# Performance work log

Measured on AMD Instinct MI355X. Metric: run time of the kernel, lower is better.

Reference implementation:

```python
import jax, jax.numpy as jnp
import numpy as np

B, T, F, U, M = 4096, 16, 256, 512, 8
DELTA_T = 0.04

# ln_tau_table: tau = 1, 10^0.5, 10^1.0, ... -> ln(tau) = i * 0.5*ln(10)
LN_TAU = (jnp.arange(M, dtype=jnp.float32) * (0.5 * np.log(10.0))).astype(jnp.float32)
DECAY = jnp.exp(-DELTA_T / (LN_TAU + 1e-7))  # [M]


def setup_inputs() -> dict:
    key = jax.random.key(0)
    ks = jax.random.split(key, 9)
    s = lambda fan_in: 1.0 / np.sqrt(fan_in)
    return {
        "x": jax.random.normal(ks[0], (B, T, F), dtype=jnp.float32),
        "W_r": jax.random.normal(ks[1], (F + U, U * M), dtype=jnp.float32) * s(F + U),
        "b_r": jax.random.normal(ks[2], (U * M,), dtype=jnp.float32) * 0.01,
        "W_q": jax.random.normal(ks[3], (F + U, U), dtype=jnp.float32) * s(F + U),
        "b_q": jax.random.normal(ks[4], (U,), dtype=jnp.float32) * 0.01,
        "W_s": jax.random.normal(ks[5], (F + U, U * M), dtype=jnp.float32) * s(F + U),
        "b_s": jax.random.normal(ks[6], (U * M,), dtype=jnp.float32) * 0.01,
        "W_out": jax.random.normal(ks[7], (U, 3), dtype=jnp.float32) * s(U),
        "b_out": jax.random.normal(ks[8], (3,), dtype=jnp.float32) * 0.01,
    }


def _ctgru_forward(x, W_r, b_r, W_q, b_q, W_s, b_s, W_out, b_out):
    def step(h_hat, x_t):  # h_hat: [B,U,M], x_t: [B,F]
        h = h_hat.sum(axis=2)                              # [B,U]
        fused = jnp.concatenate([x_t, h], axis=1)          # [B,F+U]
        ln_tau_r = (fused @ W_r + b_r).reshape(-1, U, M)   # [B,U,M]
        r_ki = jax.nn.softmax(-jnp.square(ln_tau_r - LN_TAU), axis=2)
        q_in = jnp.concatenate([x_t, jnp.sum(r_ki * h_hat, axis=2)], axis=1)
        q_k = jnp.tanh(q_in @ W_q + b_q)[:, :, None]       # [B,U,1]
        ln_tau_s = (fused @ W_s + b_s).reshape(-1, U, M)
        s_ki = jax.nn.softmax(-jnp.square(ln_tau_s - LN_TAU), axis=2)
        h_next = ((1.0 - s_ki) * h_hat + s_ki * q_k) * DECAY
        return h_next, h_next.sum(axis=2)                  # carry, hidden [B,U]

    h0 = jnp.zeros((x.shape[0], U, M), dtype=x.dtype)
    _, hiddens = jax.lax.scan(step, h0, jnp.swapaxes(x, 0, 1))  # hiddens: [T,B,U]
    outputs = jnp.swapaxes(hiddens, 0, 1)                  # [B,T,U]
    return outputs @ W_out + b_out                         # [B,T,3]


def reference(x, W_r, b_r, W_q, b_q, W_s, b_s, W_out, b_out):
    return _ctgru_forward(x, W_r, b_r, W_q, b_q, W_s, b_s, W_out, b_out)
```

## Files before the change

kernel.cpp:

```cpp
#include <hip/hip_runtime.h>
#include <hip/hip_bf16.h>
#include <math.h>

#define B_   4096
#define T_   16
#define F_   256
#define U_   512
#define M_   8
#define K_   768
#define NRS  4096
#define NC   8192
#define LNT  1.1512925f

typedef __bf16 bf16_t;
typedef bf16_t bf16x8 __attribute__((ext_vector_type(8)));
typedef bf16_t bf16x4 __attribute__((ext_vector_type(4)));
typedef float  f32x4  __attribute__((ext_vector_type(4)));

__device__ inline void gl_lds16(const void* g, void* lds) {
    __builtin_amdgcn_global_load_lds(
        (const __attribute__((address_space(1))) unsigned int*)g,
        (__attribute__((address_space(3))) unsigned int*)lds, 16, 0, 0);
}

#define VMCNT(n) asm volatile("s_waitcnt vmcnt(" #n ")" ::: "memory")
#define LGKM0()  asm volatile("s_waitcnt lgkmcnt(0)" ::: "memory")
#define BAR()    __builtin_amdgcn_s_barrier()

__device__ inline void stage_ht(const bf16_t* src, bf16_t* dst, int tid) {
    gl_lds16(src + tid * 8,        (char*)dst + tid * 16);
    gl_lds16(src + tid * 8 + 2048, (char*)dst + tid * 16 + 4096);
    gl_lds16(src + tid * 8 + 4096, (char*)dst + tid * 16 + 8192);
    gl_lds16(src + tid * 8 + 6144, (char*)dst + tid * 16 + 12288);
}

template <int IS_R>
__global__ __launch_bounds__(256, 4) void gemm_half(
    const bf16_t* __restrict__ xt_t,
    const bf16_t* __restrict__ ht,
    const bf16_t* __restrict__ Bt,
    const float*  __restrict__ biasP,
    const bf16_t* __restrict__ hhat,
    bf16_t* __restrict__ rh,
    bf16_t* __restrict__ sbuf)
{
    __shared__ __attribute__((aligned(16))) bf16_t Ah[2][8192];
    __shared__ __attribute__((aligned(16))) bf16_t Bh[2][8192];

    const int tid  = threadIdx.x;
    const int lane = tid & 63;
    const int wave = tid >> 6;

    const int lin = blockIdx.y * 32 + blockIdx.x;
    const int c = lin & 7, q = lin >> 3;
    const int mh = (c >> 1) * 8 + (q & 7);
    const int nh = (c & 1) * 16 + (q >> 3);
    const int m0 = mh * 128;
    const int NH = IS_R ? nh : 32 + nh;
    const int np = NH >> 1, nph = NH & 1;

    const int wm = wave >> 1;
    const int wn = wave & 1;
    const int lr = lane & 15;
    const int kq = lane >> 4;
    const int ck0 = (kq ^ (lr & 7)) * 8;

    f32x4 acc[4][4] = {};
    bf16x8 a[4], b[4];

#define AS(T) ((T) < 4 ? xt_t + ((size_t)((mh >> 1) * 4 + (T)) * 2 + (mh & 1)) * 8192 \
                        : ht  + ((size_t)((mh >> 1) * 8 + (T) - 4) * 2 + (mh & 1)) * 8192)
#define BS(T) (Bt + ((size_t)(np * 12 + (T)) * 2 + nph) * 8192)

#define RD(dst, base, ks) do{                                                  \
    _Pragma("unroll") for (int i = 0; i < 4; ++i)                              \
        dst[i] = *(const bf16x8*)((base) + (i * 16 + lr) * 64 + (ck0 ^ ((ks) * 32))); \
  }while(0)

#define MMA() do{ __builtin_amdgcn_s_setprio(1);                               \
    _Pragma("unroll") for (int i = 0; i < 4; ++i)                              \
      _Pragma("unroll") for (int j = 0; j < 4; ++j)                            \
        acc[i][j] = __builtin_amdgcn_mfma_f32_16x16x32_bf16(                   \
            a[i], b[j], acc[i][j], 0, 0, 0);                                   \
    __builtin_amdgcn_s_setprio(0); }while(0)

    stage_ht(AS(0), &Ah[0][0], tid);
    stage_ht(BS(0), &Bh[0][0], tid);
    VMCNT(0);
    BAR();

#define TILE(T, SFLAG)                                                         \
  {                                                                            \
    const int p_ = (T) & 1, pn_ = p_ ^ 1;                                      \
    if (SFLAG) {                                                               \
      stage_ht(AS((T) + 1), &Ah[pn_][0], tid);                                 \
      stage_ht(BS((T) + 1), &Bh[pn_][0], tid);                                 \
    }                                                                          \
    const bf16_t* Ab = &Ah[p_][0] + wm * 64 * 64;                              \
    const bf16_t* Bb = &Bh[p_][0] + wn * 64 * 64;                              \
    RD(a, Ab, 0); RD(b, Bb, 0);                                                \
    LGKM0();                                                                   \
    MMA();                                                                     \
    RD(a, Ab, 1); RD(b, Bb, 1);                                                \
    LGKM0();                                                                   \
    MMA();                                                                     \
    VMCNT(0);                                                                  \
    BAR();                                                                     \
  }

    TILE(0, 1);  TILE(1, 1);  TILE(2, 1);  TILE(3, 1);
    TILE(4, 1);  TILE(5, 1);  TILE(6, 1);  TILE(7, 1);
    TILE(8, 1);  TILE(9, 1);  TILE(10, 1); TILE(11, 0);
#undef TILE
#undef MMA
#undef RD
#undef AS
#undef BS

    const int nb  = NH * 128 + wn * 64;
    const int u3  = lane & 7;
    const int m0v = ((lane >> 3) & 1) * 4;

    float bj4[4];
#pragma unroll
    for (int j = 0; j < 4; ++j) bj4[j] = biasP[nb + j * 16 + lr];

#pragma unroll
    for (int mi = 0; mi < 4; ++mi) {
        const int rowb = m0 + wm * 64 + mi * 16 + kq * 4;
#pragma unroll
        for (int r = 0; r < 4; ++r) {
            const int row = rowb + r;
            float e[4], sum = 0.f;
#pragma unroll
            for (int j = 0; j < 4; ++j) {
                float v = acc[mi][j][r] + bj4[j];
                float d = v - (float)(m0v + j) * LNT;
                e[j] = __expf(-d * d);
                sum += e[j];
            }
            sum += __shfl_xor(sum, 8, 64);
            const float inv = 1.0f / sum;
            if (IS_R) {
                bf16x4 h4 = *(const bf16x4*)(hhat + (size_t)row * NRS + nb + u3 * 8 + m0v);
                float rhv = 0.f;
#pragma unroll
                for (int j = 0; j < 4; ++j) rhv += e[j] * inv * (float)h4[j];
                rhv += __shfl_xor(rhv, 8, 64);
                if ((lane & 8) == 0)
                    rh[(size_t)row * U_ + (nb >> 3) + u3] = (bf16_t)rhv;
            } else {
                bf16x4 pv;
#pragma unroll
                for (int j = 0; j < 4; ++j) pv[j] = (bf16_t)(e[j] * inv);
                *(bf16x4*)(sbuf + (size_t)row * NRS + (nb - NRS) + u3 * 8 + m0v) = pv;
            }
        }
    }
}

__global__ __launch_bounds__(256) void gemm_q_up(
    const bf16_t* __restrict__ xt_t,
    const bf16_t* __restrict__ rh,
    const bf16_t* __restrict__ Bqt,
    const float*  __restrict__ bq,
    const bf16_t* __restrict__ sbuf,
    bf16_t* __restrict__ hhat,
    bf16_t* __restrict__ hnext,
    bf16_t* __restrict__ htile)
{
    __shared__ __attribute__((aligned(16))) bf16_t As[4096];
    __shared__ __attribute__((aligned(16))) bf16_t Bs[4096];

    const int tid  = threadIdx.x;
    const int lane = tid & 63;
    const int wave = tid >> 6;
    const int m0 = blockIdx.x * 64;
    const int n0 = blockIdx.y * 64;
    const int wm = wave & 1;
    const int wn = wave >> 1;
    const int lr = lane & 15;
    const int kq = lane >> 4;
    const int ck0 = (kq ^ (lr & 7)) * 8;

    const int mp = m0 >> 8, half = (m0 >> 7) & 1, r0 = m0 & 127;
    const int rw = tid >> 3, q8 = tid & 7;

    f32x4 acc[2][2] = {};

    for (int kt = 0; kt < 12; ++kt) {
        __syncthreads();
        if (kt < 4) {
            const bf16_t* s = xt_t + ((size_t)(mp * 4 + kt) * 2 + half) * 8192 + r0 * 64;
            gl_lds16(s + tid * 8,        (char*)As + tid * 16);
            gl_lds16(s + tid * 8 + 2048, (char*)As + tid * 16 + 4096);
        } else {
            const int cb = (kt - 4) * 64;
            gl_lds16(rh + (size_t)(m0 + rw) * U_ + cb + ((q8 ^ (rw & 7)) * 8),
                     (char*)As + tid * 16);
            gl_lds16(rh + (size_t)(m0 + 32 + rw) * U_ + cb + ((q8 ^ (rw & 7)) * 8),
                     (char*)As + tid * 16 + 4096);
        }
        {
            const bf16_t* s = Bqt + (size_t)((n0 >> 6) * 12 + kt) * 4096;
            gl_lds16(s + tid * 8,        (char*)Bs + tid * 16);
            gl_lds16(s + tid * 8 + 2048, (char*)Bs + tid * 16 + 4096);
        }
        __syncthreads();

        bf16x8 af[4], bfr[4];
#pragma unroll
        for (int i = 0; i < 2; i++) {
            const bf16_t* pa = As + (wm * 32 + i * 16 + lr) * 64;
            const bf16_t* pb = Bs + (wn * 32 + i * 16 + lr) * 64;
            af[i * 2 + 0]  = *(const bf16x8*)(pa + ck0);
            af[i * 2 + 1]  = *(const bf16x8*)(pa + (ck0 ^ 32));
            bfr[i * 2 + 0] = *(const bf16x8*)(pb + ck0);
            bfr[i * 2 + 1] = *(const bf16x8*)(pb + (ck0 ^ 32));
        }
#pragma unroll
        for (int ks = 0; ks < 2; ks++)
#pragma unroll
            for (int i = 0; i < 2; i++)
#pragma unroll
                for (int j = 0; j < 2; j++)
                    acc[i][j] = __builtin_amdgcn_mfma_f32_16x16x32_bf16(
                        af[i * 2 + ks], bfr[j * 2 + ks], acc[i][j], 0, 0, 0);
    }

    const float DEC[8] = {0.0f, 0.9658531f, 0.9827783f, 0.9884856f,
                          0.9913518f, 0.9930754f, 0.9942261f, 0.9950489f};

#pragma unroll
    for (int i = 0; i < 2; i++) {
        const int rowb = m0 + wm * 32 + i * 16 + kq * 4;
#pragma unroll
        for (int j = 0; j < 2; j++) {
            const int u = n0 + wn * 32 + j * 16 + lr;
            const float bv = bq[u];
            const int kt2 = u >> 6, kc = u & 63;
#pragma unroll
            for (int r = 0; r < 4; r++) {
                const int row = rowb + r;
                const float qv = tanhf(acc[i][j][r] + bv);
                const size_t base = (size_t)row * NRS + u * 8;
                bf16x8 s8 = *(const bf16x8*)(sbuf + base);
                bf16x8 h8 = *(const bf16x8*)(hhat + base);
                bf16x8 ho;
                float hs = 0.f;
#pragma unroll
                for (int m = 0; m < 8; m++) {
                    float s = (float)s8[m];
                    float h = (float)h8[m];
                    float hn = ((1.f - s) * h + s * qv) * DEC[m];
                    ho[m] = (bf16_t)hn;
                    hs += hn;
                }
                *(bf16x8*)(hhat + base) = ho;
                hnext[(size_t)row * U_ + u] = (bf16_t)hs;
                htile[((((size_t)(row >> 8) * 8 + kt2) * 2 + ((row >> 7) & 1)) * 128
                       + (row & 127)) * 64
                      + (((kc >> 3) ^ (row & 7)) * 8) + (kc & 7)] = (bf16_t)hs;
            }
        }
    }
}

__global__ void transpose_perm(const float* __restrict__ src, bf16_t* __restrict__ dst) {
    __shared__ float tl[32][33];
    int k0 = blockIdx.x * 32, n0 = blockIdx.y * 32;
    int tx = threadIdx.x & 31, ty = threadIdx.x >> 5;
#pragma unroll
    for (int i = 0; i < 32; i += 8)
        tl[ty + i][tx] = src[(size_t)(k0 + ty + i) * NRS + n0 + tx];
    __syncthreads();
#pragma unroll
    for (int i = 0; i < 32; i += 8) {
        int n = n0 + ty + i;
        int m = n & 7, u3v = (n >> 3) & 7;
        int p = (n & ~63) + (m & 3) * 16 + (m >> 2) * 8 + u3v;
        dst[(size_t)p * K_ + k0 + tx] = (bf16_t)tl[tx][ty + i];
    }
}

__global__ void btile_build(const bf16_t* __restrict__ WrsT, bf16_t* __restrict__ Bt) {
    int n = blockIdx.x / 3;
    int k = (blockIdx.x % 3) * 256 + threadIdx.x;
    int np = n >> 8, rp = n & 255, hf = rp >> 7, r = rp & 127;
    int kt = k >> 6, kc = k & 63;
    Bt[((((size_t)np * 12 + kt) * 2 + hf) * 128 + r) * 64
       + (((kc >> 3) ^ (r & 7)) * 8) + (kc & 7)] = WrsT[(size_t)n * K_ + k];
}

__global__ void transpose_plain(const float* __restrict__ src, bf16_t* __restrict__ dst, int N) {
    __shared__ float tl[32][33];
    int k0 = blockIdx.x * 32, n0 = blockIdx.y * 32;
    int tx = threadIdx.x & 31, ty = threadIdx.x >> 5;
#pragma unroll
    for (int i = 0; i < 32; i += 8)
        tl[ty + i][tx] = src[(size_t)(k0 + ty + i) * N + n0 + tx];
    __syncthreads();
#pragma unroll
    for (int i = 0; i < 32; i += 8)
        dst[(size_t)(n0 + ty + i) * K_ + k0 + tx] = (bf16_t)tl[tx][ty + i];
}

__global__ void bqtile_build(const bf16_t* __restrict__ WqT, bf16_t* __restrict__ Bqt) {
    int n = blockIdx.x / 3;
    int k = (blockIdx.x % 3) * 256 + threadIdx.x;
    int np = n >> 6, r = n & 63;
    int kt = k >> 6, kc = k & 63;
    Bqt[(((size_t)np * 12 + kt) * 64 + r) * 64
        + (((kc >> 3) ^ (r & 7)) * 8) + (kc & 7)] = WqT[(size_t)n * K_ + k];
}

__global__ void bias_perm(const float* __restrict__ b_r, const float* __restrict__ b_s,
                          float* __restrict__ biasP) {
    int p = blockIdx.x * 256 + threadIdx.x;
    int pr = p & 63, j = pr >> 4, lr = pr & 15;
    int L = (p & ~63) + (lr & 7) * 8 + ((lr >> 3) & 1) * 4 + j;
    biasP[p] = (L < NRS) ? b_r[L] : b_s[L - NRS];
}

__global__ void xtile_build(const float* __restrict__ x, bf16_t* __restrict__ xt) {
    int idx = blockIdx.x * 256 + threadIdx.x;
    int b = idx >> 12;
    int rem = idx & 4095;
    int t = rem >> 8, f = rem & 255;
    int mp = b >> 8, rp = b & 255, hf = rp >> 7, r = rp & 127;
    int kt = f >> 6, kc = f & 63;
    xt[(((((size_t)t * 16 + mp) * 4 + kt) * 2 + hf) * 128 + r) * 64
       + (((kc >> 3) ^ (r & 7)) * 8) + (kc & 7)] = (bf16_t)x[idx];
}

__global__ __launch_bounds__(256) void out_all(
    const bf16_t* __restrict__ hall,
    const float* __restrict__ Wout,
    const float* __restrict__ bout,
    float* __restrict__ out)
{
    int row = blockIdx.x * 4 + (threadIdx.x >> 6);
    int lane = threadIdx.x & 63;
    bf16x8 h8 = *(const bf16x8*)(hall + (size_t)row * U_ + lane * 8);
    float p0 = 0, p1 = 0, p2 = 0;
#pragma unroll
    for (int k = 0; k < 8; k++) {
        float h = (float)h8[k];
        int u = lane * 8 + k;
        p0 += h * Wout[u * 3 + 0];
        p1 += h * Wout[u * 3 + 1];
        p2 += h * Wout[u * 3 + 2];
    }
    for (int off = 32; off; off >>= 1) {
        p0 += __shfl_down(p0, off, 64);
        p1 += __shfl_down(p1, off, 64);
        p2 += __shfl_down(p2, off, 64);
    }
    if (lane == 0) {
        int t = row >> 12, b = row & (B_ - 1);
        size_t o = ((size_t)b * T_ + t) * 3;
        out[o + 0] = p0 + bout[0];
        out[o + 1] = p1 + bout[1];
        out[o + 2] = p2 + bout[2];
    }
}

extern "C" void kernel_launch(void* const* d_in, const int* in_sizes, int n_in,
                              void* d_out, int out_size, void* d_ws, size_t ws_size,
                              hipStream_t stream) {
    const float* x   = (const float*)d_in[0];
    const float* W_r = (const float*)d_in[1];
    const float* b_r = (const float*)d_in[2];
    const float* W_q = (const float*)d_in[3];
    const float* b_q = (const float*)d_in[4];
    const float* W_s = (const float*)d_in[5];
    const float* b_s = (const float*)d_in[6];
    const float* W_o = (const float*)d_in[7];
    const float* b_o = (const float*)d_in[8];
    float* out = (float*)d_out;

    char* ws = (char*)d_ws;
    bf16_t* hhat  = (bf16_t*)ws; ws += (size_t)B_ * NRS * 2;
    bf16_t* sbuf  = (bf16_t*)ws; ws += (size_t)B_ * NRS * 2;
    bf16_t* xtile = (bf16_t*)ws; ws += (size_t)B_ * T_ * F_ * 2;
    bf16_t* hall  = (bf16_t*)ws; ws += (size_t)(T_ + 1) * B_ * U_ * 2;
    bf16_t* rh    = (bf16_t*)ws; ws += (size_t)B_ * U_ * 2;
    bf16_t* WrsT  = (bf16_t*)ws; ws += (size_t)NC * K_ * 2;
    bf16_t* Btile = (bf16_t*)ws; ws += (size_t)NC * K_ * 2;
    bf16_t* htile = (bf16_t*)ws; ws += (size_t)B_ * U_ * 2;
    bf16_t* WqT   = (bf16_t*)ws; ws += (size_t)U_ * K_ * 2;
    bf16_t* Bqtil = (bf16_t*)ws; ws += (size_t)U_ * K_ * 2;
    float*  biasP = (float*)ws;  ws += (size_t)NC * 4;

    hipMemsetAsync(hhat, 0, (size_t)B_ * NRS * 2, stream);
    hipMemsetAsync(htile, 0, (size_t)B_ * U_ * 2, stream);
    xtile_build<<<B_ * T_ * F_ / 256, 256, 0, stream>>>(x, xtile);
    transpose_perm<<<dim3(K_ / 32, NRS / 32), 256, 0, stream>>>(W_r, WrsT);
    transpose_perm<<<dim3(K_ / 32, NRS / 32), 256, 0, stream>>>(W_s, WrsT + (size_t)NRS * K_);
    btile_build<<<NC * 3, 256, 0, stream>>>(WrsT, Btile);
    transpose_plain<<<dim3(K_ / 32, U_ / 32), 256, 0, stream>>>(W_q, WqT, U_);
    bqtile_build<<<U_ * 3, 256, 0, stream>>>(WqT, Bqtil);
    bias_perm<<<NC / 256, 256, 0, stream>>>(b_r, b_s, biasP);

    for (int t = 0; t < T_; t++) {
        const bf16_t* xt_t = xtile + (size_t)t * 16 * 4 * 2 * 8192;
        bf16_t*       hn   = hall + (size_t)(t + 1) * B_ * U_;
        gemm_half<1><<<dim3(32, 32), 256, 0, stream>>>(xt_t, htile, Btile, biasP, hhat, rh, sbuf);
        gemm_half<0><<<dim3(32, 32), 256, 0, stream>>>(xt_t, htile, Btile, biasP, hhat, rh, sbuf);
        gemm_q_up<<<dim3(64, 8), 256, 0, stream>>>(xt_t, rh, Bqtil, b_q, sbuf, hhat, hn, htile);
    }
    out_all<<<B_ * T_ / 4, 256, 0, stream>>>(hall + (size_t)B_ * U_, W_o, b_o, out);
}
```

Measured before the change: 1.753 ms.

## Switch GEMM operand tiles to k-chunk-major layout with 32-wide K steps

Replaces the XOR-swizzled 128x64 row-major operand tiles with a chunk-major layout (k-chunk of 8, then row), so that the LDS reads are conflict-free without swizzling. The main gemm_half loop now stages 32-wide K slices (24 iterations, 8 KB per operand buffer instead of 16 KB), which halves LDS use but doubles the barrier count. The q GEMM, the pre-pack kernels and the htile writes are updated to match the new layout.

```diff
diff --git a/kernel.cpp b/kernel.cpp
--- a/kernel.cpp
+++ b/kernel.cpp
@@ -12,6 +12,12 @@
 #define NC   8192
 #define LNT  1.1512925f
 
+#define XPH  32768
+#define XPT  1048576
+#define HPH  65536
+#define BPH  98304
+#define QPH  49152
+
 typedef __bf16 bf16_t;
 typedef bf16_t bf16x8 __attribute__((ext_vector_type(8)));
 typedef bf16_t bf16x4 __attribute__((ext_vector_type(4)));
@@ -27,11 +33,9 @@
 #define LGKM0()  asm volatile("s_waitcnt lgkmcnt(0)" ::: "memory")
 #define BAR()    __builtin_amdgcn_s_barrier()
 
-__device__ inline void stage_ht(const bf16_t* src, bf16_t* dst, int tid) {
+__device__ inline void stage8(const bf16_t* src, bf16_t* dst, int tid) {
     gl_lds16(src + tid * 8,        (char*)dst + tid * 16);
     gl_lds16(src + tid * 8 + 2048, (char*)dst + tid * 16 + 4096);
-    gl_lds16(src + tid * 8 + 4096, (char*)dst + tid * 16 + 8192);
-    gl_lds16(src + tid * 8 + 6144, (char*)dst + tid * 16 + 12288);
 }
 
 template <int IS_R>
@@ -44,8 +48,8 @@
     bf16_t* __restrict__ rh,
     bf16_t* __restrict__ sbuf)
 {
-    __shared__ __attribute__((aligned(16))) bf16_t Ah[2][8192];
-    __shared__ __attribute__((aligned(16))) bf16_t Bh[2][8192];
+    __shared__ __attribute__((aligned(16))) bf16_t Ahl[2][4096];
+    __shared__ __attribute__((aligned(16))) bf16_t Bhl[2][4096];
 
     const int tid  = threadIdx.x;
     const int lane = tid & 63;
@@ -57,65 +61,54 @@
     const int nh = (c & 1) * 16 + (q >> 3);
     const int m0 = mh * 128;
     const int NH = IS_R ? nh : 32 + nh;
-    const int np = NH >> 1, nph = NH & 1;
 
     const int wm = wave >> 1;
     const int wn = wave & 1;
     const int lr = lane & 15;
     const int kq = lane >> 4;
-    const int ck0 = (kq ^ (lr & 7)) * 8;
+
+    const bf16_t* xp = xt_t + (size_t)mh * XPH;
+    const bf16_t* hp = ht   + (size_t)mh * HPH;
+    const bf16_t* bp = Bt   + (size_t)NH * BPH;
+
+    const int aoff = kq * 1024 + (wm * 64 + lr) * 8;
+    const int boff = kq * 1024 + (wn * 64 + lr) * 8;
 
     f32x4 acc[4][4] = {};
-    bf16x8 a[4], b[4];
-
-#define AS(T) ((T) < 4 ? xt_t + ((size_t)((mh >> 1) * 4 + (T)) * 2 + (mh & 1)) * 8192 \
-                        : ht  + ((size_t)((mh >> 1) * 8 + (T) - 4) * 2 + (mh & 1)) * 8192)
-#define BS(T) (Bt + ((size_t)(np * 12 + (T)) * 2 + nph) * 8192)
-
-#define RD(dst, base, ks) do{                                                  \
-    _Pragma("unroll") for (int i = 0; i < 4; ++i)                              \
-        dst[i] = *(const bf16x8*)((base) + (i * 16 + lr) * 64 + (ck0 ^ ((ks) * 32))); \
-  }while(0)
-
-#define MMA() do{ __builtin_amdgcn_s_setprio(1);                               \
-    _Pragma("unroll") for (int i = 0; i < 4; ++i)                              \
-      _Pragma("unroll") for (int j = 0; j < 4; ++j)                            \
-        acc[i][j] = __builtin_amdgcn_mfma_f32_16x16x32_bf16(                   \
-            a[i], b[j], acc[i][j], 0, 0, 0);                                   \
-    __builtin_amdgcn_s_setprio(0); }while(0)
-
-    stage_ht(AS(0), &Ah[0][0], tid);
-    stage_ht(BS(0), &Bh[0][0], tid);
+
+    stage8(xp, &Ahl[0][0], tid);
+    stage8(bp, &Bhl[0][0], tid);
     VMCNT(0);
     BAR();
 
-#define TILE(T, SFLAG)                                                         \
-  {                                                                            \
-    const int p_ = (T) & 1, pn_ = p_ ^ 1;                                      \
-    if (SFLAG) {                                                               \
-      stage_ht(AS((T) + 1), &Ah[pn_][0], tid);                                 \
-      stage_ht(BS((T) + 1), &Bh[pn_][0], tid);                                 \
-    }                                                                          \
-    const bf16_t* Ab = &Ah[p_][0] + wm * 64 * 64;                              \
-    const bf16_t* Bb = &Bh[p_][0] + wn * 64 * 64;                              \
-    RD(a, Ab, 0); RD(b, Bb, 0);                                                \
-    LGKM0();                                                                   \
-    MMA();                                                                     \
-    RD(a, Ab, 1); RD(b, Bb, 1);                                                \
-    LGKM0();                                                                   \
-    MMA();                                                                     \
-    VMCNT(0);                                                                  \
-    BAR();                                                                     \
-  }
-
-    TILE(0, 1);  TILE(1, 1);  TILE(2, 1);  TILE(3, 1);
-    TILE(4, 1);  TILE(5, 1);  TILE(6, 1);  TILE(7, 1);
-    TILE(8, 1);  TILE(9, 1);  TILE(10, 1); TILE(11, 0);
-#undef TILE
-#undef MMA
-#undef RD
-#undef AS
-#undef BS
+#pragma unroll
+    for (int tt = 0; tt < 24; ++tt) {
+        const int p = tt & 1, pn = p ^ 1;
+        if (tt < 23) {
+            const bf16_t* as = (tt + 1 < 8) ? xp + (tt + 1) * 4096
+                                            : hp + (tt + 1 - 8) * 4096;
+            stage8(as, &Ahl[pn][0], tid);
+            stage8(bp + (tt + 1) * 4096, &Bhl[pn][0], tid);
+        }
+        bf16x8 a[4], b[4];
+#pragma unroll
+        for (int i = 0; i < 4; ++i)
+            a[i] = *(const bf16x8*)(&Ahl[p][0] + aoff + i * 128);
+#pragma unroll
+        for (int j = 0; j < 4; ++j)
+            b[j] = *(const bf16x8*)(&Bhl[p][0] + boff + j * 128);
+        LGKM0();
+        __builtin_amdgcn_s_setprio(1);
+#pragma unroll
+        for (int i = 0; i < 4; ++i)
+#pragma unroll
+            for (int j = 0; j < 4; ++j)
+                acc[i][j] = __builtin_amdgcn_mfma_f32_16x16x32_bf16(
+                    a[i], b[j], acc[i][j], 0, 0, 0);
+        __builtin_amdgcn_s_setprio(0);
+        VMCNT(0);
+        BAR();
+    }
 
     const int nb  = NH * 128 + wn * 64;
     const int u3  = lane & 7;
@@ -181,43 +174,46 @@
     const int wn = wave >> 1;
     const int lr = lane & 15;
     const int kq = lane >> 4;
-    const int ck0 = (kq ^ (lr & 7)) * 8;
-
-    const int mp = m0 >> 8, half = (m0 >> 7) & 1, r0 = m0 & 127;
-    const int rw = tid >> 3, q8 = tid & 7;
+
+    const int chs = (tid >> 6) & 3;
+    const int rws = tid & 63;
+
+    const bf16_t* xp  = xt_t + (size_t)(m0 >> 7) * XPH;
+    const int     r0  = m0 & 127;
+    const bf16_t* bpq = Bqt + (size_t)(n0 >> 6) * QPH;
 
     f32x4 acc[2][2] = {};
 
     for (int kt = 0; kt < 12; ++kt) {
         __syncthreads();
         if (kt < 4) {
-            const bf16_t* s = xt_t + ((size_t)(mp * 4 + kt) * 2 + half) * 8192 + r0 * 64;
-            gl_lds16(s + tid * 8,        (char*)As + tid * 16);
-            gl_lds16(s + tid * 8 + 2048, (char*)As + tid * 16 + 4096);
+            gl_lds16(xp + ((size_t)((kt * 2 + 0) * 4 + chs) * 128 + r0 + rws) * 8,
+                     (char*)As + tid * 16);
+            gl_lds16(xp + ((size_t)((kt * 2 + 1) * 4 + chs) * 128 + r0 + rws) * 8,
+                     (char*)As + tid * 16 + 4096);
         } else {
             const int cb = (kt - 4) * 64;
-            gl_lds16(rh + (size_t)(m0 + rw) * U_ + cb + ((q8 ^ (rw & 7)) * 8),
+            gl_lds16(rh + (size_t)(m0 + rws) * U_ + cb + chs * 8,
                      (char*)As + tid * 16);
-            gl_lds16(rh + (size_t)(m0 + 32 + rw) * U_ + cb + ((q8 ^ (rw & 7)) * 8),
+            gl_lds16(rh + (size_t)(m0 + rws) * U_ + cb + 32 + chs * 8,
                      (char*)As + tid * 16 + 4096);
         }
-        {
-            const bf16_t* s = Bqt + (size_t)((n0 >> 6) * 12 + kt) * 4096;
-            gl_lds16(s + tid * 8,        (char*)Bs + tid * 16);
-            gl_lds16(s + tid * 8 + 2048, (char*)Bs + tid * 16 + 4096);
-        }
+        gl_lds16(bpq + ((size_t)((kt * 2 + 0) * 4 + chs) * 64 + rws) * 8,
+                 (char*)Bs + tid * 16);
+        gl_lds16(bpq + ((size_t)((kt * 2 + 1) * 4 + chs) * 64 + rws) * 8,
+                 (char*)Bs + tid * 16 + 4096);
         __syncthreads();
 
         bf16x8 af[4], bfr[4];
 #pragma unroll
-        for (int i = 0; i < 2; i++) {
-            const bf16_t* pa = As + (wm * 32 + i * 16 + lr) * 64;
-            const bf16_t* pb = Bs + (wn * 32 + i * 16 + lr) * 64;
-            af[i * 2 + 0]  = *(const bf16x8*)(pa + ck0);
-            af[i * 2 + 1]  = *(const bf16x8*)(pa + (ck0 ^ 32));
-            bfr[i * 2 + 0] = *(const bf16x8*)(pb + ck0);
-            bfr[i * 2 + 1] = *(const bf16x8*)(pb + (ck0 ^ 32));
-        }
+        for (int ks = 0; ks < 2; ks++)
+#pragma unroll
+            for (int i = 0; i < 2; i++) {
+                af[i * 2 + ks]  = *(const bf16x8*)(As +
+                    ((ks * 4 + kq) * 64 + wm * 32 + i * 16 + lr) * 8);
+                bfr[i * 2 + ks] = *(const bf16x8*)(Bs +
+                    ((ks * 4 + kq) * 64 + wn * 32 + i * 16 + lr) * 8);
+            }
 #pragma unroll
         for (int ks = 0; ks < 2; ks++)
 #pragma unroll
@@ -238,7 +234,6 @@
         for (int j = 0; j < 2; j++) {
             const int u = n0 + wn * 32 + j * 16 + lr;
             const float bv = bq[u];
-            const int kt2 = u >> 6, kc = u & 63;
 #pragma unroll
             for (int r = 0; r < 4; r++) {
                 const int row = rowb + r;
@@ -258,9 +253,8 @@
                 }
                 *(bf16x8*)(hhat + base) = ho;
                 hnext[(size_t)row * U_ + u] = (bf16_t)hs;
-                htile[((((size_t)(row >> 8) * 8 + kt2) * 2 + ((row >> 7) & 1)) * 128
-                       + (row & 127)) * 64
-                      + (((kc >> 3) ^ (row & 7)) * 8) + (kc & 7)] = (bf16_t)hs;
+                htile[((size_t)(row >> 7) * 16 + (u >> 5)) * 4096
+                      + ((((u >> 3) & 3) * 128) + (row & 127)) * 8 + (u & 7)] = (bf16_t)hs;
             }
         }
     }
@@ -286,10 +280,10 @@
 __global__ void btile_build(const bf16_t* __restrict__ WrsT, bf16_t* __restrict__ Bt) {
     int n = blockIdx.x / 3;
     int k = (blockIdx.x % 3) * 256 + threadIdx.x;
-    int np = n >> 8, rp = n & 255, hf = rp >> 7, r = rp & 127;
-    int kt = k >> 6, kc = k & 63;
-    Bt[((((size_t)np * 12 + kt) * 2 + hf) * 128 + r) * 64
-       + (((kc >> 3) ^ (r & 7)) * 8) + (kc & 7)] = WrsT[(size_t)n * K_ + k];
+    int NH = n >> 7, prow = n & 127;
+    int kt = k >> 5, ch = (k >> 3) & 3, e = k & 7;
+    Bt[(size_t)NH * BPH + (((size_t)kt * 4 + ch) * 128 + prow) * 8 + e]
+        = WrsT[(size_t)n * K_ + k];
 }
 
 __global__ void transpose_plain(const float* __restrict__ src, bf16_t* __restrict__ dst, int N) {
@@ -308,10 +302,10 @@
 __global__ void bqtile_build(const bf16_t* __restrict__ WqT, bf16_t* __restrict__ Bqt) {
     int n = blockIdx.x / 3;
     int k = (blockIdx.x % 3) * 256 + threadIdx.x;
-    int np = n >> 6, r = n & 63;
-    int kt = k >> 6, kc = k & 63;
-    Bqt[(((size_t)np * 12 + kt) * 64 + r) * 64
-        + (((kc >> 3) ^ (r & 7)) * 8) + (kc & 7)] = WqT[(size_t)n * K_ + k];
+    int np = n >> 6, prow = n & 63;
+    int kt = k >> 5, ch = (k >> 3) & 3, e = k & 7;
+    Bqt[(size_t)np * QPH + (((size_t)kt * 4 + ch) * 64 + prow) * 8 + e]
+        = WqT[(size_t)n * K_ + k];
 }
 
 __global__ void bias_perm(const float* __restrict__ b_r, const float* __restrict__ b_s,
@@ -327,10 +321,10 @@
     int b = idx >> 12;
     int rem = idx & 4095;
     int t = rem >> 8, f = rem & 255;
-    int mp = b >> 8, rp = b & 255, hf = rp >> 7, r = rp & 127;
-    int kt = f >> 6, kc = f & 63;
-    xt[(((((size_t)t * 16 + mp) * 4 + kt) * 2 + hf) * 128 + r) * 64
-       + (((kc >> 3) ^ (r & 7)) * 8) + (kc & 7)] = (bf16_t)x[idx];
+    int mh = b >> 7, prow = b & 127;
+    int kt = f >> 5, ch = (f >> 3) & 3, e = f & 7;
+    xt[(size_t)t * XPT + (size_t)mh * XPH
+       + (((size_t)kt * 4 + ch) * 128 + prow) * 8 + e] = (bf16_t)x[idx];
 }
 
 __global__ __launch_bounds__(256) void out_all(
@@ -382,18 +376,18 @@
     char* ws = (char*)d_ws;
     bf16_t* hhat  = (bf16_t*)ws; ws += (size_t)B_ * NRS * 2;
     bf16_t* sbuf  = (bf16_t*)ws; ws += (size_t)B_ * NRS * 2;
-    bf16_t* xtile = (bf16_t*)ws; ws += (size_t)B_ * T_ * F_ * 2;
+    bf16_t* xtile = (bf16_t*)ws; ws += (size_t)T_ * XPT * 2;
     bf16_t* hall  = (bf16_t*)ws; ws += (size_t)(T_ + 1) * B_ * U_ * 2;
     bf16_t* rh    = (bf16_t*)ws; ws += (size_t)B_ * U_ * 2;
     bf16_t* WrsT  = (bf16_t*)ws; ws += (size_t)NC * K_ * 2;
     bf16_t* Btile = (bf16_t*)ws; ws += (size_t)NC * K_ * 2;
-    bf16_t* htile = (bf16_t*)ws; ws += (size_t)B_ * U_ * 2;
+    bf16_t* htile = (bf16_t*)ws; ws += (size_t)32 * HPH * 2;
     bf16_t* WqT   = (bf16_t*)ws; ws += (size_t)U_ * K_ * 2;
-    bf16_t* Bqtil = (bf16_t*)ws; ws += (size_t)U_ * K_ * 2;
+    bf16_t* Bqtil = (bf16_t*)ws; ws += (size_t)8 * QPH * 2;
     float*  biasP = (float*)ws;  ws += (size_t)NC * 4;
 
     hipMemsetAsync(hhat, 0, (size_t)B_ * NRS * 2, stream);
-    hipMemsetAsync(htile, 0, (size_t)B_ * U_ * 2, stream);
+    hipMemsetAsync(htile, 0, (size_t)32 * HPH * 2, stream);
     xtile_build<<<B_ * T_ * F_ / 256, 256, 0, stream>>>(x, xtile);
     transpose_perm<<<dim3(K_ / 32, NRS / 32), 256, 0, stream>>>(W_r, WrsT);
     transpose_perm<<<dim3(K_ / 32, NRS / 32), 256, 0, stream>>>(W_s, WrsT + (size_t)NRS * K_);
@@ -403,7 +397,7 @@
     bias_perm<<<NC / 256, 256, 0, stream>>>(b_r, b_s, biasP);
 
     for (int t = 0; t < T_; t++) {
-        const bf16_t* xt_t = xtile + (size_t)t * 16 * 4 * 2 * 8192;
+        const bf16_t* xt_t = xtile + (size_t)t * XPT;
         bf16_t*       hn   = hall + (size_t)(t + 1) * B_ * U_;
         gemm_half<1><<<dim3(32, 32), 256, 0, stream>>>(xt_t, htile, Btile, biasP, hhat, rh, sbuf);
         gemm_half<0><<<dim3(32, 32), 256, 0, stream>>>(xt_t, htile, Btile, biasP, hhat, rh, sbuf);
```

Result: faster. 1.496 ms (-14.7%).
